# Kernel tuning notes

Measured on AMD Instinct MI355X. Metric: run time of the kernel, lower is better.

## Reference

```python
import jax, jax.numpy as jnp
import numpy as np

C, W, H = 16, 48, 48
OUTDIMS = 4000
COMPONENTS = 1
BATCH = 128
EPS = 1e-6
INIT_NOISE = 1e-3


def setup_inputs() -> dict:
    key = jax.random.key(0)
    kx, kw, kh, kf = jax.random.split(key, 4)
    x = jax.random.normal(kx, (BATCH, C, W, H), dtype=jnp.float32)
    width = jax.random.normal(kw, (OUTDIMS, 1, W, 1, COMPONENTS), dtype=jnp.float32) * INIT_NOISE
    height = jax.random.normal(kh, (OUTDIMS, 1, 1, H, COMPONENTS), dtype=jnp.float32) * INIT_NOISE
    features = jax.random.normal(kf, (OUTDIMS, C, 1, 1), dtype=jnp.float32) * INIT_NOISE
    bias = jnp.zeros((OUTDIMS,), dtype=jnp.float32)
    return {"x": x, "width": width, "height": height, "features": features, "bias": bias}


def reference(x, width, height, features, bias):
    # normalize width over the w axis (dim 2), height over the h axis (dim 3)
    wn = width / jnp.sqrt(jnp.sum(width * width, axis=2, keepdims=True) + EPS)
    hn = height / jnp.sqrt(jnp.sum(height * height, axis=3, keepdims=True) + EPS)
    # spatial mask: sum of outer products over components -> (outdims, w, h)
    spatial = jnp.sum(wn * hn, axis=4)[:, 0]  # broadcast (n,1,w,1,k)*(n,1,1,h,k)
    feat = features[:, :, 0, 0]  # (outdims, c)
    # y[b,n] = sum_{c,w,h} x[b,c,w,h] * spatial[n,w,h] * feat[n,c]  (same math as
    # x.view(N,-1) @ weight.t() where weight = spatial * features, flattened cwh)
    y = jnp.einsum('bcwh,nwh,nc->bn', x, spatial, feat)
    return y + bias[None, :]
```

## Files before the change

### kernel.cpp

```cpp
#include <hip/hip_runtime.h>
#include <stdint.h>

#define OUTD 4000
#define NPAD 4096
#define CC 16
#define WW 48
#define HH 48
#define BB 128
#define KD 768
#define MD 6144
#define EPSF 1e-6f

#define BM 192
#define BNB 256
#define BKU 32
#define UNITS 24
#define AELEMS (BM * BKU)
#define SLOT_ELEMS ((BM + BNB) * BKU)
#define THREADS 256
#define XPB 2304

using short8 = __attribute__((ext_vector_type(8))) short;
using f32x4  = __attribute__((ext_vector_type(4))) float;

static __device__ __forceinline__ unsigned short f2bf(float f) {
  union { float f; unsigned int u; } v; v.f = f;
  unsigned int u = v.u;
  unsigned int r = (u + 0x7FFFu + ((u >> 16) & 1u)) >> 16;
  return (unsigned short)r;
}

__global__ __launch_bounds__(256)
void prep_all(const float* __restrict__ x,
              const float* __restrict__ width,
              const float* __restrict__ height,
              const float* __restrict__ feat,
              unsigned short* __restrict__ A,
              unsigned short* __restrict__ Qt,
              float* __restrict__ wnT) {
  __shared__ float smw[4][WW];
  int bid = blockIdx.x;
  if (bid < XPB) {
    int t = bid * 256 + threadIdx.x;
    int e = t * 8;
    int h0 = e % HH;
    int w = (e / HH) % WW;
    int c = (e / (HH * WW)) % CC;
    int b = e / (HH * WW * CC);
    float4 v0 = *(const float4*)(x + e);
    float4 v1 = *(const float4*)(x + e + 4);
    short8 o;
    o[0] = (short)f2bf(v0.x); o[1] = (short)f2bf(v0.y);
    o[2] = (short)f2bf(v0.z); o[3] = (short)f2bf(v0.w);
    o[4] = (short)f2bf(v1.x); o[5] = (short)f2bf(v1.y);
    o[6] = (short)f2bf(v1.z); o[7] = (short)f2bf(v1.w);
    *(short8*)&A[(size_t)(b * WW + w) * KD + c * HH + h0] = o;
  } else {
    int lane = threadIdx.x & 63;
    int wv = threadIdx.x >> 6;
    int nbase = (bid - XPB) * 4;
    int n = nbase + wv;
    bool valid = (n < OUTD);
    float hv = (valid && lane < HH) ? height[n * HH + lane] : 0.f;
    float wvv = (valid && lane < WW) ? width[n * WW + lane] : 0.f;
    float hs = hv * hv, wsum = wvv * wvv;
    #pragma unroll
    for (int off = 32; off > 0; off >>= 1) {
      hs += __shfl_xor(hs, off);
      wsum += __shfl_xor(wsum, off);
    }
    float hnorm = rsqrtf(hs + EPSF);
    float wnorm = rsqrtf(wsum + EPSF);
    if (lane < WW) smw[wv][lane] = wvv * wnorm;
    if (valid) {
      #pragma unroll
      for (int i = lane; i < KD; i += 64) {
        int c = i / HH, h = i % HH;
        Qt[(size_t)n * KD + i] = f2bf(feat[n * CC + c] * height[n * HH + h] * hnorm);
      }
    } else {
      #pragma unroll
      for (int i = lane; i < KD; i += 64) Qt[(size_t)n * KD + i] = 0;
    }
    __syncthreads();
    if (threadIdx.x < WW) {
      int w = threadIdx.x;
      float4 o = make_float4(smw[0][w], smw[1][w], smw[2][w], smw[3][w]);
      *(float4*)&wnT[w * NPAD + nbase] = o;
    }
  }
}

__global__ __launch_bounds__(THREADS, 2)
void gemm_main(const unsigned short* __restrict__ A,
               const unsigned short* __restrict__ Qt,
               const float* __restrict__ wnT,
               const float* __restrict__ bias,
               float* __restrict__ out) {
  __shared__ unsigned short S[2 * SLOT_ELEMS];

  int tid = threadIdx.x;
  int lane = tid & 63;
  int wid = tid >> 6;
  int wm = wid >> 1;
  int wn = wid & 1;

  int bid = blockIdx.x;
  int xcd = bid & 7;
  int i = bid >> 3;
  int by = xcd * 4 + (i & 3);
  int bxg = i >> 2;
  int n0 = bxg * BNB;
  int m0 = by * BM;

  int lrow = lane >> 2;
  int g = lane & 3;
  int gsw = (g ^ ((lrow >> 1) & 3)) * 8;
  const unsigned short* gsrc[7];
  int ldst[7];
  #pragma unroll
  for (int j = 0; j < 3; ++j) {
    int c = wid * 3 + j;
    gsrc[j] = A + (size_t)(m0 + c * 16 + lrow) * KD + gsw;
    ldst[j] = c * 512;
  }
  #pragma unroll
  for (int j = 0; j < 4; ++j) {
    int c = wid * 4 + j;
    gsrc[3 + j] = Qt + (size_t)(n0 + c * 16 + lrow) * KD + gsw;
    ldst[3 + j] = AELEMS + c * 512;
  }

#define SLOTB(u) (((u) & 1) * SLOT_ELEMS)
#define STAGE(u)                                                                  \
  { _Pragma("unroll")                                                             \
    for (int j = 0; j < 7; ++j)                                                   \
      __builtin_amdgcn_global_load_lds(                                           \
          (const __attribute__((address_space(1))) void*)(gsrc[j] + (u) * BKU),   \
          (__attribute__((address_space(3))) void*)(&S[SLOTB(u) + ldst[j]]), 16, 0, 0); }

  int q16 = lane & 15;
  int hi = lane >> 4;
  int kgr = (hi ^ ((q16 >> 1) & 3)) * 8;
  int arow = (wm * 96 + q16) * BKU + kgr;
  int brow = AELEMS + (wn * 128 + q16) * BKU + kgr;

  f32x4 acc[6][8] = {};
  short8 af[6];
  short8 bf[4];

  STAGE(0);

  #pragma unroll
  for (int u = 0; u < UNITS; ++u) {
    if (u + 1 < UNITS) {
      STAGE(u + 1);
      asm volatile("s_waitcnt vmcnt(7)" ::: "memory");
    } else {
      asm volatile("s_waitcnt vmcnt(0)" ::: "memory");
    }
    __builtin_amdgcn_s_barrier();
    __builtin_amdgcn_sched_barrier(0);

    const unsigned short* sb = &S[SLOTB(u)];
    #pragma unroll
    for (int mi = 0; mi < 6; ++mi)
      af[mi] = *(const short8*)&sb[arow + mi * 512];
    #pragma unroll
    for (int ni = 0; ni < 4; ++ni)
      bf[ni] = *(const short8*)&sb[brow + ni * 512];
    asm volatile("s_waitcnt lgkmcnt(0)" ::: "memory");
    __builtin_amdgcn_sched_barrier(0);
    __builtin_amdgcn_s_setprio(1);
    #pragma unroll
    for (int ni = 0; ni < 4; ++ni)
      #pragma unroll
      for (int mi = 0; mi < 6; ++mi)
        acc[mi][ni] = __builtin_amdgcn_mfma_f32_16x16x32_bf16(af[mi], bf[ni], acc[mi][ni], 0, 0, 0);
    __builtin_amdgcn_s_setprio(0);
    #pragma unroll
    for (int ni = 0; ni < 4; ++ni)
      bf[ni] = *(const short8*)&sb[brow + (4 + ni) * 512];
    asm volatile("s_waitcnt lgkmcnt(0)" ::: "memory");
    __builtin_amdgcn_sched_barrier(0);
    __builtin_amdgcn_s_setprio(1);
    #pragma unroll
    for (int ni = 0; ni < 4; ++ni)
      #pragma unroll
      for (int mi = 0; mi < 6; ++mi)
        acc[mi][4 + ni] = __builtin_amdgcn_mfma_f32_16x16x32_bf16(af[mi], bf[ni], acc[mi][4 + ni], 0, 0, 0);
    __builtin_amdgcn_s_setprio(0);
    __builtin_amdgcn_sched_barrier(0);
  }

  int b0 = by * 4 + wm * 2;
  #pragma unroll
  for (int ni = 0; ni < 8; ++ni) {
    int ng = n0 + wn * 128 + ni * 16 + q16;
    float s0 = 0.f, s1 = 0.f;
    #pragma unroll
    for (int mi = 0; mi < 3; ++mi) {
      int wbase = mi * 16 + hi * 4;
      f32x4 va = acc[mi][ni];
      f32x4 vb = acc[mi + 3][ni];
      #pragma unroll
      for (int r = 0; r < 4; ++r) {
        float t = wnT[(wbase + r) * NPAD + ng];
        s0 += t * va[r];
        s1 += t * vb[r];
      }
    }
    s0 += __shfl_xor(s0, 16); s0 += __shfl_xor(s0, 32);
    s1 += __shfl_xor(s1, 16); s1 += __shfl_xor(s1, 32);
    if (hi == 0 && ng < OUTD) {
      float bv = bias[ng];
      out[(size_t)b0 * OUTD + ng] = s0 + bv;
      out[(size_t)(b0 + 1) * OUTD + ng] = s1 + bv;
    }
  }
#undef STAGE
#undef SLOTB
}

extern "C" void kernel_launch(void* const* d_in, const int* in_sizes, int n_in,
                              void* d_out, int out_size, void* d_ws, size_t ws_size,
                              hipStream_t stream) {
  const float* x      = (const float*)d_in[0];
  const float* width  = (const float*)d_in[1];
  const float* height = (const float*)d_in[2];
  const float* feat   = (const float*)d_in[3];
  const float* bias   = (const float*)d_in[4];
  float* out = (float*)d_out;

  char* ws = (char*)d_ws;
  unsigned short* A  = (unsigned short*)ws;
  unsigned short* Qt = (unsigned short*)(ws + 9437184);
  float* wnT         = (float*)(ws + 9437184 + 6291456);

  prep_all<<<dim3(XPB + NPAD / 4), dim3(256), 0, stream>>>(x, width, height, feat, A, Qt, wnT);
  gemm_main<<<dim3(512), dim3(THREADS), 0, stream>>>(A, Qt, wnT, bias, out);
}
```

Baseline: 54.68 us.

## Deepen GEMM pipeline to 4-stage LDS ring with 8 waves and register double-buffering

```diff
diff --git a/kernel.cpp b/kernel.cpp
--- a/kernel.cpp
+++ b/kernel.cpp
@@ -17,7 +17,7 @@
 #define UNITS 24
 #define AELEMS (BM * BKU)
 #define SLOT_ELEMS ((BM + BNB) * BKU)
-#define THREADS 256
+#define THREADS 512
 #define XPB 2304
 
 using short8 = __attribute__((ext_vector_type(8))) short;
@@ -97,13 +97,13 @@
                const float* __restrict__ wnT,
                const float* __restrict__ bias,
                float* __restrict__ out) {
-  __shared__ unsigned short S[2 * SLOT_ELEMS];
+  __shared__ unsigned short S[4 * SLOT_ELEMS];
 
   int tid = threadIdx.x;
   int lane = tid & 63;
   int wid = tid >> 6;
-  int wm = wid >> 1;
-  int wn = wid & 1;
+  int wm = wid >> 2;
+  int wn = wid & 3;
 
   int bid = blockIdx.x;
   int xcd = bid & 7;
@@ -116,87 +116,104 @@
   int lrow = lane >> 2;
   int g = lane & 3;
   int gsw = (g ^ ((lrow >> 1) & 3)) * 8;
-  const unsigned short* gsrc[7];
-  int ldst[7];
-  #pragma unroll
-  for (int j = 0; j < 3; ++j) {
-    int c = wid * 3 + j;
-    gsrc[j] = A + (size_t)(m0 + c * 16 + lrow) * KD + gsw;
-    ldst[j] = c * 512;
-  }
+  const int cbase[8] = {0, 4, 7, 11, 14, 18, 21, 25};
+  const int clen[8]  = {4, 3, 4, 3, 4, 3, 4, 3};
+  int base = cbase[wid];
+  int nl = clen[wid];
+  const unsigned short* gp[4];
+  int ldst[4];
   #pragma unroll
   for (int j = 0; j < 4; ++j) {
-    int c = wid * 4 + j;
-    gsrc[3 + j] = Qt + (size_t)(n0 + c * 16 + lrow) * KD + gsw;
-    ldst[3 + j] = AELEMS + c * 512;
-  }
-
-#define SLOTB(u) (((u) & 1) * SLOT_ELEMS)
-#define STAGE(u)                                                                  \
+    int c = base + (j < nl ? j : nl - 1);
+    gp[j] = (c < 12 ? A + (size_t)(m0 + c * 16 + lrow) * KD
+                    : Qt + (size_t)(n0 + (c - 12) * 16 + lrow) * KD) + gsw;
+    ldst[j] = c * 512;
+  }
+
+#define SLOTB(u) (((u) & 3) * SLOT_ELEMS)
+#define STAGE_P1(u)                                                               \
   { _Pragma("unroll")                                                             \
-    for (int j = 0; j < 7; ++j)                                                   \
+    for (int j = 0; j < 2; ++j)                                                   \
       __builtin_amdgcn_global_load_lds(                                           \
-          (const __attribute__((address_space(1))) void*)(gsrc[j] + (u) * BKU),   \
+          (const __attribute__((address_space(1))) void*)(gp[j] + (u) * BKU),     \
           (__attribute__((address_space(3))) void*)(&S[SLOTB(u) + ldst[j]]), 16, 0, 0); }
+#define STAGE_P2(u)                                                               \
+  { _Pragma("unroll")                                                             \
+    for (int j = 2; j < 4; ++j)                                                   \
+      if (j < nl)                                                                 \
+        __builtin_amdgcn_global_load_lds(                                         \
+            (const __attribute__((address_space(1))) void*)(gp[j] + (u) * BKU),   \
+            (__attribute__((address_space(3))) void*)(&S[SLOTB(u) + ldst[j]]), 16, 0, 0); }
 
   int q16 = lane & 15;
   int hi = lane >> 4;
   int kgr = (hi ^ ((q16 >> 1) & 3)) * 8;
   int arow = (wm * 96 + q16) * BKU + kgr;
-  int brow = AELEMS + (wn * 128 + q16) * BKU + kgr;
-
-  f32x4 acc[6][8] = {};
-  short8 af[6];
-  short8 bf[4];
-
-  STAGE(0);
+  int brow = AELEMS + (wn * 64 + q16) * BKU + kgr;
+
+  f32x4 acc[6][4] = {};
+  short8 af[2][6];
+  short8 bf[2][4];
+
+#define DSREAD_P1(set, u)                                               \
+  { const unsigned short* sb = &S[SLOTB(u)];                            \
+    _Pragma("unroll")                                                   \
+    for (int mi = 0; mi < 6; ++mi)                                      \
+      af[set][mi] = *(const short8*)&sb[arow + mi * 512];               \
+    bf[set][0] = *(const short8*)&sb[brow];                             \
+    bf[set][1] = *(const short8*)&sb[brow + 512]; }
+#define DSREAD_BF23(set, u)                                             \
+  { const unsigned short* sb = &S[SLOTB(u)];                            \
+    bf[set][2] = *(const short8*)&sb[brow + 1024];                      \
+    bf[set][3] = *(const short8*)&sb[brow + 1536]; }
+#define MFMA12(set, nlo)                                                \
+  { _Pragma("unroll")                                                   \
+    for (int ni = (nlo); ni < (nlo) + 2; ++ni)                          \
+      _Pragma("unroll")                                                 \
+      for (int mi = 0; mi < 6; ++mi)                                    \
+        acc[mi][ni] = __builtin_amdgcn_mfma_f32_16x16x32_bf16(af[set][mi], bf[set][ni], acc[mi][ni], 0, 0, 0); }
+
+  STAGE_P1(0); STAGE_P2(0);
+  STAGE_P1(1); STAGE_P2(1);
+  STAGE_P1(2); STAGE_P2(2);
+  asm volatile("s_waitcnt vmcnt(6)" ::: "memory");
+  __builtin_amdgcn_s_barrier();
+  __builtin_amdgcn_sched_barrier(0);
+  DSREAD_P1(0, 0);
+  __builtin_amdgcn_sched_barrier(0);
 
   #pragma unroll
   for (int u = 0; u < UNITS; ++u) {
+    const int cs = u & 1, ns = cs ^ 1;
+    if (u + 3 < UNITS) STAGE_P1(u + 3);
+    DSREAD_BF23(cs, u);
+    asm volatile("s_waitcnt lgkmcnt(2)" ::: "memory");
+    __builtin_amdgcn_sched_barrier(0);
+    __builtin_amdgcn_s_setprio(1);
+    MFMA12(cs, 0);
+    __builtin_amdgcn_s_setprio(0);
+    __builtin_amdgcn_sched_barrier(0);
+    if (u + 3 < UNITS) STAGE_P2(u + 3);
+    if (u + 3 < UNITS)      asm volatile("s_waitcnt vmcnt(6) lgkmcnt(0)" ::: "memory");
+    else if (u + 2 < UNITS) asm volatile("s_waitcnt vmcnt(3) lgkmcnt(0)" ::: "memory");
+    else if (u + 1 < UNITS) asm volatile("s_waitcnt vmcnt(0) lgkmcnt(0)" ::: "memory");
+    else                    asm volatile("s_waitcnt lgkmcnt(0)" ::: "memory");
+    __builtin_amdgcn_sched_barrier(0);
     if (u + 1 < UNITS) {
-      STAGE(u + 1);
-      asm volatile("s_waitcnt vmcnt(7)" ::: "memory");
-    } else {
-      asm volatile("s_waitcnt vmcnt(0)" ::: "memory");
-    }
-    __builtin_amdgcn_s_barrier();
-    __builtin_amdgcn_sched_barrier(0);
-
-    const unsigned short* sb = &S[SLOTB(u)];
-    #pragma unroll
-    for (int mi = 0; mi < 6; ++mi)
-      af[mi] = *(const short8*)&sb[arow + mi * 512];
-    #pragma unroll
-    for (int ni = 0; ni < 4; ++ni)
-      bf[ni] = *(const short8*)&sb[brow + ni * 512];
-    asm volatile("s_waitcnt lgkmcnt(0)" ::: "memory");
+      __builtin_amdgcn_s_barrier();
+      DSREAD_P1(ns, u + 1);
+    }
     __builtin_amdgcn_sched_barrier(0);
     __builtin_amdgcn_s_setprio(1);
-    #pragma unroll
-    for (int ni = 0; ni < 4; ++ni)
-      #pragma unroll
-      for (int mi = 0; mi < 6; ++mi)
-        acc[mi][ni] = __builtin_amdgcn_mfma_f32_16x16x32_bf16(af[mi], bf[ni], acc[mi][ni], 0, 0, 0);
-    __builtin_amdgcn_s_setprio(0);
-    #pragma unroll
-    for (int ni = 0; ni < 4; ++ni)
-      bf[ni] = *(const short8*)&sb[brow + (4 + ni) * 512];
-    asm volatile("s_waitcnt lgkmcnt(0)" ::: "memory");
-    __builtin_amdgcn_sched_barrier(0);
-    __builtin_amdgcn_s_setprio(1);
-    #pragma unroll
-    for (int ni = 0; ni < 4; ++ni)
-      #pragma unroll
-      for (int mi = 0; mi < 6; ++mi)
-        acc[mi][4 + ni] = __builtin_amdgcn_mfma_f32_16x16x32_bf16(af[mi], bf[ni], acc[mi][4 + ni], 0, 0, 0);
+    MFMA12(cs, 2);
     __builtin_amdgcn_s_setprio(0);
     __builtin_amdgcn_sched_barrier(0);
   }
 
   int b0 = by * 4 + wm * 2;
   #pragma unroll
-  for (int ni = 0; ni < 8; ++ni) {
-    int ng = n0 + wn * 128 + ni * 16 + q16;
+  for (int ni = 0; ni < 4; ++ni) {
+    int ng = n0 + wn * 64 + ni * 16 + q16;
     float s0 = 0.f, s1 = 0.f;
     #pragma unroll
     for (int mi = 0; mi < 3; ++mi) {
@@ -218,8 +235,12 @@
       out[(size_t)(b0 + 1) * OUTD + ng] = s1 + bv;
     }
   }
-#undef STAGE
 #undef SLOTB
+#undef STAGE_P1
+#undef STAGE_P2
+#undef DSREAD_P1
+#undef DSREAD_BF23
+#undef MFMA12
 }
 
 extern "C" void kernel_launch(void* const* d_in, const int* in_sizes, int n_in,
```

After: 51.28 us. -6.2%, faster.
